# Performance work log

Measured on AMD Instinct MI355X. Metric: run time of the kernel, lower is better.

Reference implementation:

```python
import jax, jax.numpy as jnp
import numpy as np

HEADS = 20
NUM_AOE = 16
NUM_IP = 16


def setup_inputs() -> dict:
    key = jax.random.key(0)
    ks = jax.random.split(key, 7)
    B, Sq, H = 8, 4096, 1280
    Skv, C = 109, 768
    scale = 0.02
    return {
        "hidden_states": jax.random.normal(ks[0], (B, Sq, H), jnp.float32),
        "encoder_hidden_states": jax.random.normal(ks[1], (B, Skv, C), jnp.float32),
        "Wq": jax.random.normal(ks[2], (H, H), jnp.float32) * scale,
        "Wk": jax.random.normal(ks[3], (C, H), jnp.float32) * scale,
        "Wv": jax.random.normal(ks[4], (C, H), jnp.float32) * scale,
        "Wo": jax.random.normal(ks[5], (H, H), jnp.float32) * scale,
        "bo": jnp.zeros((H,), jnp.float32),
    }


def reference(hidden_states, encoder_hidden_states, Wq, Wk, Wv, Wo, bo):
    B, Sq, H = hidden_states.shape
    Skv = encoder_hidden_states.shape[1]
    head_dim = H // HEADS
    residual = hidden_states

    # projections (no bias on q/k/v, as in diffusers SD attention)
    q = (hidden_states @ Wq).reshape(B, Sq, HEADS, head_dim).transpose(0, 2, 1, 3)
    k = (encoder_hidden_states @ Wk).reshape(B, Skv, HEADS, head_dim).transpose(0, 2, 1, 3)
    v = (encoder_hidden_states @ Wv).reshape(B, Skv, HEADS, head_dim).transpose(0, 2, 1, 3)

    # manual attention: QK^T / sqrt(d), softmax
    scores = jnp.einsum("bhqd,bhkd->bhqk", q, k) / jnp.sqrt(jnp.asarray(head_dim, q.dtype))
    probs = jax.nn.softmax(scores, axis=-1)

    # frequency_mode != 'both': rescale aoe (first NUM_AOE) and image (last NUM_IP)
    # key-token ranges post-softmax, then renormalize. scale_aoe = scale_ip = 1
    # in this config, but the renormalization math is kept faithfully.
    scale_aoe = jnp.asarray(1.0, probs.dtype)
    scale_ip = jnp.asarray(1.0, probs.dtype)
    idx = jnp.arange(Skv)
    scale_vector = jnp.where(idx < NUM_AOE, scale_aoe, 1.0)
    scale_vector = jnp.where(idx >= Skv - NUM_IP, scale_vector * scale_ip, scale_vector)
    probs = probs * scale_vector  # broadcasts over (B, HEADS, Sq, Skv)
    probs = probs / probs.sum(axis=-1, keepdims=True)

    out = jnp.einsum("bhqk,bhkd->bhqd", probs, v)
    out = out.transpose(0, 2, 1, 3).reshape(B, Sq, H)
    out = out @ Wo + bo
    # residual connection, rescale_output_factor = 1.0
    return out + residual
```

## Files before the change

kernel.cpp:

```cpp
#include <hip/hip_runtime.h>
#include <hip/hip_bf16.h>

typedef unsigned short u16;
typedef __attribute__((ext_vector_type(8))) short short8;
typedef __attribute__((ext_vector_type(4))) short short4v;
typedef __attribute__((ext_vector_type(4))) float f32x4;

#define HEADS 20
#define HD 64
#define BB 8
#define SQ 4096
#define HDIM 1280
#define SKV 109
#define CDIM 768
#define SKV_PAD 128
#define SKV_T 112

static __device__ __forceinline__ u16 f2bf(float x) {
  union { __hip_bfloat16 h; u16 u; } cv;
  cv.h = __float2bfloat16(x);
  return cv.u;
}

static __device__ __forceinline__ void gll16(const void* g, void* l) {
  __builtin_amdgcn_global_load_lds(
      (const __attribute__((address_space(1))) unsigned int*)g,
      (__attribute__((address_space(3))) unsigned int*)l, 16, 0, 0);
}

__global__ __launch_bounds__(256) void tcvt(const float* __restrict__ W,
                                            u16* __restrict__ out, int K, int N,
                                            float scale) {
  __shared__ float t[32][33];
  int tx = threadIdx.x & 31, ty = threadIdx.x >> 5;
  int n0 = blockIdx.x * 32, k0 = blockIdx.y * 32;
#pragma unroll
  for (int i = 0; i < 32; i += 8)
    t[ty + i][tx] = W[(size_t)(k0 + ty + i) * N + n0 + tx];
  __syncthreads();
#pragma unroll
  for (int i = 0; i < 32; i += 8)
    out[(size_t)(n0 + ty + i) * K + k0 + tx] = f2bf(t[tx][ty + i] * scale);
}

__global__ __launch_bounds__(256) void ehs_prep(const float* __restrict__ e,
                                                u16* __restrict__ out) {
  int idx = blockIdx.x * 256 + threadIdx.x;
  if (idx >= BB * SKV_PAD * CDIM / 4) return;
  int c4 = idx * 4;
  int b = c4 / (SKV_PAD * CDIM);
  int rem = c4 - b * (SKV_PAD * CDIM);
  int s = rem / CDIM;
  int c = rem - s * CDIM;
  short4v o = {0, 0, 0, 0};
  if (s < SKV) {
    f32x4 v = *(const f32x4*)(e + ((size_t)b * SKV + s) * CDIM + c);
#pragma unroll
    for (int j = 0; j < 4; j++) o[j] = (short)f2bf(v[j]);
  }
  *(short4v*)&out[c4] = o;
}

__global__ __launch_bounds__(256) void hscvt(const float* __restrict__ in,
                                             u16* __restrict__ out) {
  const size_t total = (size_t)BB * SQ * HDIM;
  size_t step = (size_t)gridDim.x * 256 * 8;
  for (size_t i = ((size_t)blockIdx.x * 256 + threadIdx.x) * 8; i < total;
       i += step) {
    f32x4 a = *(const f32x4*)(in + i);
    f32x4 b = *(const f32x4*)(in + i + 4);
    short8 o;
#pragma unroll
    for (int j = 0; j < 4; j++) {
      o[j] = (short)f2bf(a[j]);
      o[j + 4] = (short)f2bf(b[j]);
    }
    *(short8*)&out[i] = o;
  }
}

template <int MODE>
__global__ __launch_bounds__(256, 4)
void gemm_glds(const u16* __restrict__ A, const u16* __restrict__ Bt,
               void* __restrict__ outp, int K, int ntn,
               const float* __restrict__ bias, const float* __restrict__ resid) {
  __shared__ u16 Alds[128 * 32];
  __shared__ u16 Blds[128 * 32];
  const int tid = threadIdx.x;
  const int wid = tid >> 6, lane = tid & 63;
  const int wm = wid >> 1, wn = wid & 1;
  const int g = lane >> 4, r = lane & 15;

  const int nwg = gridDim.x;
  const int orig = blockIdx.x;
  const int wg = (orig & 7) * (nwg >> 3) + (orig >> 3);
  const int mt = wg / ntn, nt = wg - mt * ntn;
  const int row0 = mt * 128, col0 = nt * 128;

  const int erow = tid >> 2, ecol = (tid & 3) * 8;

  f32x4 acc[4][4] = {};

  for (int kt = 0; kt < K; kt += 32) {
    const u16* ag = A + (size_t)(row0 + erow) * K + kt + ecol;
    const u16* bg = Bt + (size_t)(col0 + erow) * K + kt + ecol;
    gll16(ag, &Alds[erow * 32 + ecol]);
    gll16(ag + (size_t)64 * K, &Alds[(erow + 64) * 32 + ecol]);
    gll16(bg, &Blds[erow * 32 + ecol]);
    gll16(bg + (size_t)64 * K, &Blds[(erow + 64) * 32 + ecol]);
    __syncthreads();

    short8 afr[4], bfr[4];
#pragma unroll
    for (int mi = 0; mi < 4; mi++)
      afr[mi] = *(short8*)&Alds[(wm * 64 + mi * 16 + r) * 32 + g * 8];
#pragma unroll
    for (int ni = 0; ni < 4; ni++)
      bfr[ni] = *(short8*)&Blds[(wn * 64 + ni * 16 + r) * 32 + g * 8];
#pragma unroll
    for (int mi = 0; mi < 4; mi++)
#pragma unroll
      for (int ni = 0; ni < 4; ni++)
        acc[mi][ni] = __builtin_amdgcn_mfma_f32_16x16x32_bf16(afr[mi], bfr[ni],
                                                              acc[mi][ni], 0, 0, 0);
    __syncthreads();
  }

  if constexpr (MODE == 0) {
    u16* O = (u16*)outp;
#pragma unroll
    for (int mi = 0; mi < 4; mi++)
#pragma unroll
      for (int i = 0; i < 4; i++) {
        size_t m = row0 + wm * 64 + mi * 16 + g * 4 + i;
        size_t base = m * HDIM + col0 + wn * 64 + r;
#pragma unroll
        for (int ni = 0; ni < 4; ni++)
          O[base + ni * 16] = f2bf(acc[mi][ni][i]);
      }
  } else if constexpr (MODE == 1 || MODE == 2) {
    u16* O = (u16*)outp;
#pragma unroll
    for (int mi = 0; mi < 4; mi++)
#pragma unroll
      for (int i = 0; i < 4; i++) {
        int m = row0 + wm * 64 + mi * 16 + g * 4 + i;
        int b = m >> 7, skv = m & 127;
#pragma unroll
        for (int ni = 0; ni < 4; ni++) {
          int col = col0 + wn * 64 + ni * 16 + r;
          int hh = col >> 6, d = col & 63;
          size_t addr;
          if constexpr (MODE == 1)
            addr = (((size_t)b * HEADS + hh) * SKV_PAD + skv) * HD + d;
          else
            addr = (((size_t)b * HEADS + hh) * HD + d) * SKV_PAD + skv;
          O[addr] = f2bf(acc[mi][ni][i]);
        }
      }
  } else {
    float* O = (float*)outp;
#pragma unroll
    for (int mi = 0; mi < 4; mi++)
#pragma unroll
      for (int i = 0; i < 4; i++) {
        size_t m = row0 + wm * 64 + mi * 16 + g * 4 + i;
        size_t base = m * HDIM + col0 + wn * 64 + r;
#pragma unroll
        for (int ni = 0; ni < 4; ni++) {
          int col = col0 + wn * 64 + ni * 16 + r;
          O[base + ni * 16] = acc[mi][ni][i] + bias[col] + resid[base + ni * 16];
        }
      }
  }
}

__global__ __launch_bounds__(256, 2)
void attn_kernel(const u16* __restrict__ q, const u16* __restrict__ kh,
                 const u16* __restrict__ vt, u16* __restrict__ o) {
  __shared__ u16 Klds[SKV_T * 72];
  __shared__ u16 Vlds[HD * 136];
  __shared__ u16 Plds[4 * 16 * 136];
  const int tid = threadIdx.x;
  const int wid = tid >> 6, lane = tid & 63;
  const int g = lane >> 4, r = lane & 15;
  const int qt = blockIdx.x;
  const int bh = blockIdx.y;
  const int b = bh / HEADS, h = bh - b * HEADS;

  const u16* kg = kh + (size_t)bh * SKV_PAD * HD;
  for (int i = tid; i < SKV_T * 8; i += 256) {
    int row = i >> 3, c = (i & 7) * 8;
    *(short8*)&Klds[row * 72 + c] = *(const short8*)(kg + row * HD + c);
  }
  const u16* vg = vt + (size_t)bh * HD * SKV_PAD;
  for (int i = tid; i < HD * 16; i += 256) {
    int row = i >> 4, c = (i & 15) * 8;
    *(short8*)&Vlds[row * 136 + c] = *(const short8*)(vg + row * SKV_PAD + c);
  }
  __syncthreads();

  const u16* qg = q + ((size_t)b * SQ + qt * 64 + wid * 16 + r) * HDIM + h * HD + g * 8;
  short8 aq0 = *(const short8*)(qg);
  short8 aq1 = *(const short8*)(qg + 32);

  f32x4 s[7];
#pragma unroll
  for (int nf = 0; nf < 7; nf++) {
    f32x4 z = {0.f, 0.f, 0.f, 0.f};
    short8 k0 = *(short8*)&Klds[(nf * 16 + r) * 72 + g * 8];
    short8 k1 = *(short8*)&Klds[(nf * 16 + r) * 72 + 32 + g * 8];
    z = __builtin_amdgcn_mfma_f32_16x16x32_bf16(aq0, k0, z, 0, 0, 0);
    z = __builtin_amdgcn_mfma_f32_16x16x32_bf16(aq1, k1, z, 0, 0, 0);
    s[nf] = z;
  }

  {
    short4v z = {0, 0, 0, 0};
    *(short4v*)&Plds[(wid * 16 + r) * 136 + 112 + g * 4] = z;
  }

#pragma unroll
  for (int i = 0; i < 4; i++) {
    float pv[7];
    float mx = -1e30f;
#pragma unroll
    for (int nf = 0; nf < 7; nf++) {
      float v = s[nf][i];
      if (nf == 6 && r >= 13) v = -1e30f;
      pv[nf] = v;
      mx = fmaxf(mx, v);
    }
#pragma unroll
    for (int d = 1; d < 16; d <<= 1) mx = fmaxf(mx, __shfl_xor(mx, d, 64));
    float sum = 0.f;
#pragma unroll
    for (int nf = 0; nf < 7; nf++) {
      float e = (nf == 6 && r >= 13) ? 0.f : __expf(pv[nf] - mx);
      pv[nf] = e;
      sum += e;
    }
#pragma unroll
    for (int d = 1; d < 16; d <<= 1) sum += __shfl_xor(sum, d, 64);
    float is = 1.f / sum;
#pragma unroll
    for (int nf = 0; nf < 7; nf++)
      Plds[(wid * 16 + g * 4 + i) * 136 + nf * 16 + r] = f2bf(pv[nf] * is);
  }
  __syncthreads();

  f32x4 oacc[4] = {};
#pragma unroll
  for (int kk = 0; kk < 4; kk++) {
    short8 ap = *(short8*)&Plds[(wid * 16 + r) * 136 + kk * 32 + g * 8];
#pragma unroll
    for (int nf = 0; nf < 4; nf++) {
      short8 bv = *(short8*)&Vlds[(nf * 16 + r) * 136 + kk * 32 + g * 8];
      oacc[nf] = __builtin_amdgcn_mfma_f32_16x16x32_bf16(ap, bv, oacc[nf], 0, 0, 0);
    }
  }
  u16* og = o + ((size_t)b * SQ + qt * 64 + wid * 16) * HDIM + h * HD;
#pragma unroll
  for (int nf = 0; nf < 4; nf++)
#pragma unroll
    for (int i = 0; i < 4; i++)
      og[(size_t)(g * 4 + i) * HDIM + nf * 16 + r] = f2bf(oacc[nf][i]);
}

extern "C" void kernel_launch(void* const* d_in, const int* in_sizes, int n_in,
                              void* d_out, int out_size, void* d_ws, size_t ws_size,
                              hipStream_t stream) {
  const float* hs  = (const float*)d_in[0];
  const float* ehs = (const float*)d_in[1];
  const float* Wq  = (const float*)d_in[2];
  const float* Wk  = (const float*)d_in[3];
  const float* Wv  = (const float*)d_in[4];
  const float* Wo  = (const float*)d_in[5];
  const float* bo  = (const float*)d_in[6];

  char* ws = (char*)d_ws;
  size_t off = 0;
  auto alloc = [&](size_t elems) {
    u16* p = (u16*)(ws + off);
    off += ((elems * 2 + 255) / 256) * 256;
    return p;
  };
  u16* wqt  = alloc((size_t)HDIM * HDIM);
  u16* wot  = alloc((size_t)HDIM * HDIM);
  u16* wkt  = alloc((size_t)HDIM * CDIM);
  u16* wvt  = alloc((size_t)HDIM * CDIM);
  u16* ehsp = alloc((size_t)BB * SKV_PAD * CDIM);
  u16* khb  = alloc((size_t)BB * HEADS * SKV_PAD * HD);
  u16* vtb  = alloc((size_t)BB * HEADS * HD * SKV_PAD);
  u16* qb   = alloc((size_t)BB * SQ * HDIM);
  u16* ao   = alloc((size_t)BB * SQ * HDIM);
  u16* hsb  = ao;

  tcvt<<<dim3(HDIM / 32, HDIM / 32), 256, 0, stream>>>(Wq, wqt, HDIM, HDIM, 0.125f);
  tcvt<<<dim3(HDIM / 32, CDIM / 32), 256, 0, stream>>>(Wk, wkt, CDIM, HDIM, 1.0f);
  tcvt<<<dim3(HDIM / 32, CDIM / 32), 256, 0, stream>>>(Wv, wvt, CDIM, HDIM, 1.0f);
  tcvt<<<dim3(HDIM / 32, HDIM / 32), 256, 0, stream>>>(Wo, wot, HDIM, HDIM, 1.0f);
  ehs_prep<<<dim3((BB * SKV_PAD * CDIM / 4 + 255) / 256), 256, 0, stream>>>(ehs, ehsp);
  hscvt<<<dim3(2048), 256, 0, stream>>>(hs, hsb);

  gemm_glds<1><<<dim3(80), 256, 0, stream>>>(ehsp, wkt, khb, CDIM, 10, nullptr, nullptr);
  gemm_glds<2><<<dim3(80), 256, 0, stream>>>(ehsp, wvt, vtb, CDIM, 10, nullptr, nullptr);
  gemm_glds<0><<<dim3(2560), 256, 0, stream>>>(hsb, wqt, qb, HDIM, 10, nullptr, nullptr);
  attn_kernel<<<dim3(SQ / 64, BB * HEADS), 256, 0, stream>>>(qb, khb, vtb, ao);
  gemm_glds<3><<<dim3(2560), 256, 0, stream>>>(ao, wot, (void*)d_out, HDIM, 10, bo, hs);
}
```

Baseline: 486.7 us.

## Replace large Q/O projections with 256x256 double-buffered pipelined GEMM

Adds a new 512-thread GEMM kernel with 256x256 output tiles, K-step 64, XOR-swizzled LDS and double buffering. Global-to-LDS loads for the next tile are interleaved with four MFMA quadrants, using s_setprio around the math blocks. It is used for the Q projection and the output projection with bias and residual, while the small K/V projections keep the old kernel. The aim is more data reuse per tile and hiding memory latency behind MFMA work, at the cost of fewer workgroups (640) and higher register and LDS pressure.

```diff
diff --git a/kernel.cpp b/kernel.cpp
--- a/kernel.cpp
+++ b/kernel.cpp
@@ -15,6 +15,8 @@
 #define CDIM 768
 #define SKV_PAD 128
 #define SKV_T 112
+
+#define SBAR() asm volatile("s_barrier" ::: "memory")
 
 static __device__ __forceinline__ u16 f2bf(float x) {
   union { __hip_bfloat16 h; u16 u; } cv;
@@ -79,11 +81,183 @@
   }
 }
 
+
+static __device__ __forceinline__ void stage_half(u16* region,
+                                                  const u16* gbase, int K,
+                                                  int tid) {
+#pragma unroll
+  for (int j = 0; j < 2; ++j) {
+    int c = tid + j * 512;
+    int s = c ^ ((c >> 3) & 7);
+    gll16(gbase + (size_t)(s >> 3) * K + (s & 7) * 8, region + c * 8);
+  }
+}
+
+static __device__ __forceinline__ short8 lread(const u16* region, int row,
+                                               int kcol) {
+  int idx = (row * 64 + kcol) ^ ((row & 7) << 3);
+  return *(const short8*)(region + idx);
+}
+
+template <int MODE>
+__global__ __launch_bounds__(512, 2)
+void gemm256(const u16* __restrict__ A, const u16* __restrict__ Bt,
+             void* __restrict__ outp, int K, int ntn,
+             const float* __restrict__ bias, const float* __restrict__ resid) {
+  __shared__ u16 lds[2][2][2][8192];
+  const int tid = threadIdx.x;
+  const int wid = tid >> 6, lane = tid & 63;
+  const int wm = wid >> 2, wn = wid & 3;
+  const int g = lane >> 4, r = lane & 15;
+
+  const int nwg = gridDim.x;
+  const int orig = blockIdx.x;
+  const int wg = (orig & 7) * (nwg >> 3) + (orig >> 3);
+  const int mt = wg / ntn, nt = wg - mt * ntn;
+  const int row0 = mt * 256, col0 = nt * 256;
+
+  const u16* Ag = A + (size_t)row0 * K;
+  const u16* Bg = Bt + (size_t)col0 * K;
+  const int NT = K >> 6;
+
+  f32x4 acc[8][4] = {};
+
+  stage_half(&lds[0][0][0][0], Ag, K, tid);
+  stage_half(&lds[0][0][1][0], Ag + (size_t)128 * K, K, tid);
+  stage_half(&lds[0][1][0][0], Bg, K, tid);
+  stage_half(&lds[0][1][1][0], Bg + (size_t)128 * K, K, tid);
+  stage_half(&lds[1][1][0][0], Bg + 64, K, tid);
+  stage_half(&lds[1][1][1][0], Bg + (size_t)128 * K + 64, K, tid);
+  asm volatile("s_waitcnt vmcnt(4)" ::: "memory");
+  SBAR();
+
+  for (int t = 0; t < NT; ++t) {
+    const int cur = t & 1, nxt = cur ^ 1;
+    const u16* Ac = &lds[cur][0][wm][0];
+    const u16* Bc = &lds[cur][1][wn >> 1][0];
+    const int brow = (wn & 1) * 64;
+    short8 a0[4][2], a1[4][2], b0[2][2], b1[2][2];
+
+#pragma unroll
+    for (int mi = 0; mi < 4; ++mi)
+#pragma unroll
+      for (int ks = 0; ks < 2; ++ks)
+        a0[mi][ks] = lread(Ac, mi * 16 + r, ks * 32 + g * 8);
+#pragma unroll
+    for (int nf = 0; nf < 2; ++nf)
+#pragma unroll
+      for (int ks = 0; ks < 2; ++ks)
+        b0[nf][ks] = lread(Bc, brow + nf * 16 + r, ks * 32 + g * 8);
+    if (t + 1 < NT)
+      stage_half(&lds[nxt][0][0][0], Ag + (size_t)(t + 1) * 64, K, tid);
+    SBAR();
+    __builtin_amdgcn_s_setprio(1);
+#pragma unroll
+    for (int mi = 0; mi < 4; ++mi)
+#pragma unroll
+      for (int nf = 0; nf < 2; ++nf)
+#pragma unroll
+        for (int ks = 0; ks < 2; ++ks)
+          acc[mi][nf] = __builtin_amdgcn_mfma_f32_16x16x32_bf16(
+              a0[mi][ks], b0[nf][ks], acc[mi][nf], 0, 0, 0);
+    __builtin_amdgcn_s_setprio(0);
+    SBAR();
+
+#pragma unroll
+    for (int nf = 0; nf < 2; ++nf)
+#pragma unroll
+      for (int ks = 0; ks < 2; ++ks)
+        b1[nf][ks] = lread(Bc, brow + 32 + nf * 16 + r, ks * 32 + g * 8);
+    if (t + 1 < NT)
+      stage_half(&lds[nxt][0][1][0], Ag + (size_t)128 * K + (size_t)(t + 1) * 64,
+                 K, tid);
+    SBAR();
+    __builtin_amdgcn_s_setprio(1);
+#pragma unroll
+    for (int mi = 0; mi < 4; ++mi)
+#pragma unroll
+      for (int nf = 0; nf < 2; ++nf)
+#pragma unroll
+        for (int ks = 0; ks < 2; ++ks)
+          acc[mi][2 + nf] = __builtin_amdgcn_mfma_f32_16x16x32_bf16(
+              a0[mi][ks], b1[nf][ks], acc[mi][2 + nf], 0, 0, 0);
+    __builtin_amdgcn_s_setprio(0);
+    SBAR();
+
+#pragma unroll
+    for (int mi = 0; mi < 4; ++mi)
+#pragma unroll
+      for (int ks = 0; ks < 2; ++ks)
+        a1[mi][ks] = lread(Ac, 64 + mi * 16 + r, ks * 32 + g * 8);
+    if (t + 2 < NT)
+      stage_half(&lds[cur][1][0][0], Bg + (size_t)(t + 2) * 64, K, tid);
+    SBAR();
+    __builtin_amdgcn_s_setprio(1);
+#pragma unroll
+    for (int mi = 0; mi < 4; ++mi)
+#pragma unroll
+      for (int nf = 0; nf < 2; ++nf)
+#pragma unroll
+        for (int ks = 0; ks < 2; ++ks)
+          acc[4 + mi][2 + nf] = __builtin_amdgcn_mfma_f32_16x16x32_bf16(
+              a1[mi][ks], b1[nf][ks], acc[4 + mi][2 + nf], 0, 0, 0);
+    __builtin_amdgcn_s_setprio(0);
+    SBAR();
+
+    if (t + 2 < NT)
+      stage_half(&lds[cur][1][1][0], Bg + (size_t)128 * K + (size_t)(t + 2) * 64,
+                 K, tid);
+    if (t < NT - 2)
+      asm volatile("s_waitcnt vmcnt(4)" ::: "memory");
+    else
+      asm volatile("s_waitcnt vmcnt(0)" ::: "memory");
+    SBAR();
+    __builtin_amdgcn_s_setprio(1);
+#pragma unroll
+    for (int mi = 0; mi < 4; ++mi)
+#pragma unroll
+      for (int nf = 0; nf < 2; ++nf)
+#pragma unroll
+        for (int ks = 0; ks < 2; ++ks)
+          acc[4 + mi][nf] = __builtin_amdgcn_mfma_f32_16x16x32_bf16(
+              a1[mi][ks], b0[nf][ks], acc[4 + mi][nf], 0, 0, 0);
+    __builtin_amdgcn_s_setprio(0);
+    SBAR();
+  }
+
+  if constexpr (MODE == 0) {
+    u16* O = (u16*)outp;
+#pragma unroll
+    for (int am = 0; am < 8; ++am)
+#pragma unroll
+      for (int i = 0; i < 4; ++i) {
+        size_t m = row0 + wm * 128 + am * 16 + g * 4 + i;
+        size_t base = m * HDIM + col0 + wn * 64 + r;
+#pragma unroll
+        for (int an = 0; an < 4; ++an)
+          O[base + an * 16] = f2bf(acc[am][an][i]);
+      }
+  } else {
+    float* O = (float*)outp;
+#pragma unroll
+    for (int am = 0; am < 8; ++am)
+#pragma unroll
+      for (int i = 0; i < 4; ++i) {
+        size_t m = row0 + wm * 128 + am * 16 + g * 4 + i;
+        size_t base = m * HDIM + col0 + wn * 64 + r;
+#pragma unroll
+        for (int an = 0; an < 4; ++an) {
+          int col = col0 + wn * 64 + an * 16 + r;
+          O[base + an * 16] = acc[am][an][i] + bias[col] + resid[base + an * 16];
+        }
+      }
+  }
+}
+
 template <int MODE>
 __global__ __launch_bounds__(256, 4)
 void gemm_glds(const u16* __restrict__ A, const u16* __restrict__ Bt,
-               void* __restrict__ outp, int K, int ntn,
-               const float* __restrict__ bias, const float* __restrict__ resid) {
+               void* __restrict__ outp, int K, int ntn) {
   __shared__ u16 Alds[128 * 32];
   __shared__ u16 Blds[128 * 32];
   const int tid = threadIdx.x;
@@ -96,7 +270,6 @@
   const int wg = (orig & 7) * (nwg >> 3) + (orig >> 3);
   const int mt = wg / ntn, nt = wg - mt * ntn;
   const int row0 = mt * 128, col0 = nt * 128;
-
   const int erow = tid >> 2, ecol = (tid & 3) * 8;
 
   f32x4 acc[4][4] = {};
@@ -126,53 +299,25 @@
     __syncthreads();
   }
 
-  if constexpr (MODE == 0) {
-    u16* O = (u16*)outp;
-#pragma unroll
-    for (int mi = 0; mi < 4; mi++)
-#pragma unroll
-      for (int i = 0; i < 4; i++) {
-        size_t m = row0 + wm * 64 + mi * 16 + g * 4 + i;
-        size_t base = m * HDIM + col0 + wn * 64 + r;
-#pragma unroll
-        for (int ni = 0; ni < 4; ni++)
-          O[base + ni * 16] = f2bf(acc[mi][ni][i]);
+  u16* O = (u16*)outp;
+#pragma unroll
+  for (int mi = 0; mi < 4; mi++)
+#pragma unroll
+    for (int i = 0; i < 4; i++) {
+      int m = row0 + wm * 64 + mi * 16 + g * 4 + i;
+      int b = m >> 7, skv = m & 127;
+#pragma unroll
+      for (int ni = 0; ni < 4; ni++) {
+        int col = col0 + wn * 64 + ni * 16 + r;
+        int hh = col >> 6, d = col & 63;
+        size_t addr;
+        if constexpr (MODE == 1)
+          addr = (((size_t)b * HEADS + hh) * SKV_PAD + skv) * HD + d;
+        else
+          addr = (((size_t)b * HEADS + hh) * HD + d) * SKV_PAD + skv;
+        O[addr] = f2bf(acc[mi][ni][i]);
       }
-  } else if constexpr (MODE == 1 || MODE == 2) {
-    u16* O = (u16*)outp;
-#pragma unroll
-    for (int mi = 0; mi < 4; mi++)
-#pragma unroll
-      for (int i = 0; i < 4; i++) {
-        int m = row0 + wm * 64 + mi * 16 + g * 4 + i;
-        int b = m >> 7, skv = m & 127;
-#pragma unroll
-        for (int ni = 0; ni < 4; ni++) {
-          int col = col0 + wn * 64 + ni * 16 + r;
-          int hh = col >> 6, d = col & 63;
-          size_t addr;
-          if constexpr (MODE == 1)
-            addr = (((size_t)b * HEADS + hh) * SKV_PAD + skv) * HD + d;
-          else
-            addr = (((size_t)b * HEADS + hh) * HD + d) * SKV_PAD + skv;
-          O[addr] = f2bf(acc[mi][ni][i]);
-        }
-      }
-  } else {
-    float* O = (float*)outp;
-#pragma unroll
-    for (int mi = 0; mi < 4; mi++)
-#pragma unroll
-      for (int i = 0; i < 4; i++) {
-        size_t m = row0 + wm * 64 + mi * 16 + g * 4 + i;
-        size_t base = m * HDIM + col0 + wn * 64 + r;
-#pragma unroll
-        for (int ni = 0; ni < 4; ni++) {
-          int col = col0 + wn * 64 + ni * 16 + r;
-          O[base + ni * 16] = acc[mi][ni][i] + bias[col] + resid[base + ni * 16];
-        }
-      }
-  }
+    }
 }
 
 __global__ __launch_bounds__(256, 2)
@@ -303,9 +448,9 @@
   ehs_prep<<<dim3((BB * SKV_PAD * CDIM / 4 + 255) / 256), 256, 0, stream>>>(ehs, ehsp);
   hscvt<<<dim3(2048), 256, 0, stream>>>(hs, hsb);
 
-  gemm_glds<1><<<dim3(80), 256, 0, stream>>>(ehsp, wkt, khb, CDIM, 10, nullptr, nullptr);
-  gemm_glds<2><<<dim3(80), 256, 0, stream>>>(ehsp, wvt, vtb, CDIM, 10, nullptr, nullptr);
-  gemm_glds<0><<<dim3(2560), 256, 0, stream>>>(hsb, wqt, qb, HDIM, 10, nullptr, nullptr);
+  gemm_glds<1><<<dim3(80), 256, 0, stream>>>(ehsp, wkt, khb, CDIM, 10);
+  gemm_glds<2><<<dim3(80), 256, 0, stream>>>(ehsp, wvt, vtb, CDIM, 10);
+  gemm256<0><<<dim3(640), 512, 0, stream>>>(hsb, wqt, qb, HDIM, 5, nullptr, nullptr);
   attn_kernel<<<dim3(SQ / 64, BB * HEADS), 256, 0, stream>>>(qb, khb, vtb, ao);
-  gemm_glds<3><<<dim3(2560), 256, 0, stream>>>(ao, wot, (void*)d_out, HDIM, 10, bo, hs);
-}
+  gemm256<3><<<dim3(640), 512, 0, stream>>>(ao, wot, (void*)d_out, HDIM, 5, bo, hs);
+}
```

Result: faster. 464.1 us (-4.6%).

## Add triple-buffered swizzled LDS GEMM for Q and output projections

Applied to the files above, without the earlier changes.

Introduces gemm_tb, a GEMM kernel that prefetches three K-tiles into LDS with global_load_lds, waits with partial vmcnt, and uses an XOR swizzle on LDS columns to reduce bank conflicts. It also raises wave priority around the MFMA block. The Q projection and output projection (with bias and residual) now use it, while the K/V projections keep the old single-buffered kernel, which is trimmed to its MODE 1/2 epilogues. The aim is to hide global load latency behind MFMA work. The cost is more LDS per block (48 KB), which may limit occupancy, plus redundant loads of tile 0 issued in the final iterations.

```diff
diff --git a/kernel.cpp b/kernel.cpp
--- a/kernel.cpp
+++ b/kernel.cpp
@@ -16,6 +16,8 @@
 #define SKV_PAD 128
 #define SKV_T 112
 
+#define SBAR() asm volatile("s_barrier" ::: "memory")
+
 static __device__ __forceinline__ u16 f2bf(float x) {
   union { __hip_bfloat16 h; u16 u; } cv;
   cv.h = __float2bfloat16(x);
@@ -26,6 +28,12 @@
   __builtin_amdgcn_global_load_lds(
       (const __attribute__((address_space(1))) unsigned int*)g,
       (__attribute__((address_space(3))) unsigned int*)l, 16, 0, 0);
+}
+
+static __device__ __forceinline__ short8 ldsr(unsigned addr) {
+  short8 d;
+  asm volatile("ds_read_b128 %0, %1" : "=v"(d) : "v"(addr));
+  return d;
 }
 
 __global__ __launch_bounds__(256) void tcvt(const float* __restrict__ W,
@@ -79,11 +87,119 @@
   }
 }
 
+
+static __device__ __forceinline__ void stage128(u16* __restrict__ Ar,
+                                                u16* __restrict__ Br,
+                                                const u16* __restrict__ Ag,
+                                                const u16* __restrict__ Bg,
+                                                int K, int kt, int tid) {
+#pragma unroll
+  for (int j = 0; j < 2; ++j) {
+    int c = tid + j * 256;
+    int row = c >> 2, gc = c & 3;
+    int sc = gc ^ ((row >> 1) & 3);
+    gll16(Ag + (size_t)row * K + kt + sc * 8, Ar + c * 8);
+    gll16(Bg + (size_t)row * K + kt + sc * 8, Br + c * 8);
+  }
+}
+
+template <int MODE>
+__global__ __launch_bounds__(256, 4)
+void gemm_tb(const u16* __restrict__ A, const u16* __restrict__ Bt,
+             void* __restrict__ outp, int K, int ntn,
+             const float* __restrict__ bias, const float* __restrict__ resid) {
+  __shared__ u16 lds[3][8192];
+  const int tid = threadIdx.x;
+  const int wid = tid >> 6, lane = tid & 63;
+  const int wm = wid >> 1, wn = wid & 1;
+  const int g = lane >> 4, r = lane & 15;
+
+  const int nwg = gridDim.x;
+  const int orig = blockIdx.x;
+  const int wg = (orig & 7) * (nwg >> 3) + (orig >> 3);
+  const int mt = wg / ntn, nt = wg - mt * ntn;
+  const int row0 = mt * 128, col0 = nt * 128;
+
+  const u16* Ag = A + (size_t)row0 * K;
+  const u16* Bg = Bt + (size_t)col0 * K;
+  const int NT = K >> 5;
+
+  const int cx = (g * 8) ^ (((r >> 1) & 3) << 3);
+  const unsigned lbase = (unsigned)(size_t)(
+      __attribute__((address_space(3))) u16*)&lds[0][0];
+  unsigned aoff[4], boff[4];
+#pragma unroll
+  for (int mi = 0; mi < 4; ++mi)
+    aoff[mi] = ((wm * 64 + mi * 16 + r) * 32 + cx) * 2;
+#pragma unroll
+  for (int ni = 0; ni < 4; ++ni)
+    boff[ni] = (4096 + (wn * 64 + ni * 16 + r) * 32 + cx) * 2;
+
+  f32x4 acc[4][4] = {};
+
+  stage128(&lds[0][0], &lds[0][4096], Ag, Bg, K, 0, tid);
+  stage128(&lds[1][0], &lds[1][4096], Ag, Bg, K, 32, tid);
+  stage128(&lds[2][0], &lds[2][4096], Ag, Bg, K, 64, tid);
+
+  int buf = 0;
+  for (int t = 0; t < NT; ++t) {
+    asm volatile("s_waitcnt vmcnt(8)" ::: "memory");
+    SBAR();
+    const unsigned base = lbase + buf * 16384u;
+    short8 a[4], b[4];
+#pragma unroll
+    for (int mi = 0; mi < 4; ++mi) a[mi] = ldsr(base + aoff[mi]);
+#pragma unroll
+    for (int ni = 0; ni < 4; ++ni) b[ni] = ldsr(base + boff[ni]);
+    asm volatile("s_waitcnt lgkmcnt(0)" ::: "memory");
+    __builtin_amdgcn_sched_barrier(0);
+    __builtin_amdgcn_s_setprio(1);
+#pragma unroll
+    for (int mi = 0; mi < 4; ++mi)
+#pragma unroll
+      for (int ni = 0; ni < 4; ++ni)
+        acc[mi][ni] = __builtin_amdgcn_mfma_f32_16x16x32_bf16(a[mi], b[ni],
+                                                              acc[mi][ni], 0, 0, 0);
+    __builtin_amdgcn_s_setprio(0);
+    SBAR();
+    const int kt3 = (t + 3 < NT) ? (t + 3) * 32 : 0;
+    stage128(&lds[buf][0], &lds[buf][4096], Ag, Bg, K, kt3, tid);
+    buf = (buf == 2) ? 0 : buf + 1;
+  }
+
+  if constexpr (MODE == 0) {
+    u16* O = (u16*)outp;
+#pragma unroll
+    for (int mi = 0; mi < 4; ++mi)
+#pragma unroll
+      for (int i = 0; i < 4; ++i) {
+        size_t m = row0 + wm * 64 + mi * 16 + g * 4 + i;
+        size_t base = m * HDIM + col0 + wn * 64 + r;
+#pragma unroll
+        for (int ni = 0; ni < 4; ++ni)
+          O[base + ni * 16] = f2bf(acc[mi][ni][i]);
+      }
+  } else {
+    float* O = (float*)outp;
+#pragma unroll
+    for (int mi = 0; mi < 4; ++mi)
+#pragma unroll
+      for (int i = 0; i < 4; ++i) {
+        size_t m = row0 + wm * 64 + mi * 16 + g * 4 + i;
+        size_t base = m * HDIM + col0 + wn * 64 + r;
+#pragma unroll
+        for (int ni = 0; ni < 4; ++ni) {
+          int col = col0 + wn * 64 + ni * 16 + r;
+          O[base + ni * 16] = acc[mi][ni][i] + bias[col] + resid[base + ni * 16];
+        }
+      }
+  }
+}
+
 template <int MODE>
 __global__ __launch_bounds__(256, 4)
 void gemm_glds(const u16* __restrict__ A, const u16* __restrict__ Bt,
-               void* __restrict__ outp, int K, int ntn,
-               const float* __restrict__ bias, const float* __restrict__ resid) {
+               void* __restrict__ outp, int K, int ntn) {
   __shared__ u16 Alds[128 * 32];
   __shared__ u16 Blds[128 * 32];
   const int tid = threadIdx.x;
@@ -96,7 +212,6 @@
   const int wg = (orig & 7) * (nwg >> 3) + (orig >> 3);
   const int mt = wg / ntn, nt = wg - mt * ntn;
   const int row0 = mt * 128, col0 = nt * 128;
-
   const int erow = tid >> 2, ecol = (tid & 3) * 8;
 
   f32x4 acc[4][4] = {};
@@ -126,53 +241,25 @@
     __syncthreads();
   }
 
-  if constexpr (MODE == 0) {
-    u16* O = (u16*)outp;
-#pragma unroll
-    for (int mi = 0; mi < 4; mi++)
-#pragma unroll
-      for (int i = 0; i < 4; i++) {
-        size_t m = row0 + wm * 64 + mi * 16 + g * 4 + i;
-        size_t base = m * HDIM + col0 + wn * 64 + r;
-#pragma unroll
-        for (int ni = 0; ni < 4; ni++)
-          O[base + ni * 16] = f2bf(acc[mi][ni][i]);
+  u16* O = (u16*)outp;
+#pragma unroll
+  for (int mi = 0; mi < 4; mi++)
+#pragma unroll
+    for (int i = 0; i < 4; i++) {
+      int m = row0 + wm * 64 + mi * 16 + g * 4 + i;
+      int b = m >> 7, skv = m & 127;
+#pragma unroll
+      for (int ni = 0; ni < 4; ni++) {
+        int col = col0 + wn * 64 + ni * 16 + r;
+        int hh = col >> 6, d = col & 63;
+        size_t addr;
+        if constexpr (MODE == 1)
+          addr = (((size_t)b * HEADS + hh) * SKV_PAD + skv) * HD + d;
+        else
+          addr = (((size_t)b * HEADS + hh) * HD + d) * SKV_PAD + skv;
+        O[addr] = f2bf(acc[mi][ni][i]);
       }
-  } else if constexpr (MODE == 1 || MODE == 2) {
-    u16* O = (u16*)outp;
-#pragma unroll
-    for (int mi = 0; mi < 4; mi++)
-#pragma unroll
-      for (int i = 0; i < 4; i++) {
-        int m = row0 + wm * 64 + mi * 16 + g * 4 + i;
-        int b = m >> 7, skv = m & 127;
-#pragma unroll
-        for (int ni = 0; ni < 4; ni++) {
-          int col = col0 + wn * 64 + ni * 16 + r;
-          int hh = col >> 6, d = col & 63;
-          size_t addr;
-          if constexpr (MODE == 1)
-            addr = (((size_t)b * HEADS + hh) * SKV_PAD + skv) * HD + d;
-          else
-            addr = (((size_t)b * HEADS + hh) * HD + d) * SKV_PAD + skv;
-          O[addr] = f2bf(acc[mi][ni][i]);
-        }
-      }
-  } else {
-    float* O = (float*)outp;
-#pragma unroll
-    for (int mi = 0; mi < 4; mi++)
-#pragma unroll
-      for (int i = 0; i < 4; i++) {
-        size_t m = row0 + wm * 64 + mi * 16 + g * 4 + i;
-        size_t base = m * HDIM + col0 + wn * 64 + r;
-#pragma unroll
-        for (int ni = 0; ni < 4; ni++) {
-          int col = col0 + wn * 64 + ni * 16 + r;
-          O[base + ni * 16] = acc[mi][ni][i] + bias[col] + resid[base + ni * 16];
-        }
-      }
-  }
+    }
 }
 
 __global__ __launch_bounds__(256, 2)
@@ -303,9 +390,9 @@
   ehs_prep<<<dim3((BB * SKV_PAD * CDIM / 4 + 255) / 256), 256, 0, stream>>>(ehs, ehsp);
   hscvt<<<dim3(2048), 256, 0, stream>>>(hs, hsb);
 
-  gemm_glds<1><<<dim3(80), 256, 0, stream>>>(ehsp, wkt, khb, CDIM, 10, nullptr, nullptr);
-  gemm_glds<2><<<dim3(80), 256, 0, stream>>>(ehsp, wvt, vtb, CDIM, 10, nullptr, nullptr);
-  gemm_glds<0><<<dim3(2560), 256, 0, stream>>>(hsb, wqt, qb, HDIM, 10, nullptr, nullptr);
+  gemm_glds<1><<<dim3(80), 256, 0, stream>>>(ehsp, wkt, khb, CDIM, 10);
+  gemm_glds<2><<<dim3(80), 256, 0, stream>>>(ehsp, wvt, vtb, CDIM, 10);
+  gemm_tb<0><<<dim3(2560), 256, 0, stream>>>(hsb, wqt, qb, HDIM, 10, nullptr, nullptr);
   attn_kernel<<<dim3(SQ / 64, BB * HEADS), 256, 0, stream>>>(qb, khb, vtb, ao);
-  gemm_glds<3><<<dim3(2560), 256, 0, stream>>>(ao, wot, (void*)d_out, HDIM, 10, bo, hs);
-}
+  gemm_tb<3><<<dim3(2560), 256, 0, stream>>>(ao, wot, (void*)d_out, HDIM, 10, bo, hs);
+}
```

Result: slower. 499.7 us (+2.7%).

## Add triple-buffered swizzled 128x256 GEMM for Q and output projections

Applied to the files above, without the earlier changes.

Adds a new gemm_v2 kernel with 512 threads, a 128x256 output tile, a three-stage LDS ring filled by global_load_lds, and XOR-swizzled LDS addressing. It waits with explicit vmcnt counts and raw s_barrier instead of syncthreads, and raises wave priority around the MFMA block. The aim is to overlap global loads with MFMA work and cut LDS bank conflicts in the two large GEMMs. The old gemm_glds is trimmed to the K/V modes only. The larger tile halves the grid and raises LDS use per block, which may reduce occupancy.

```diff
diff --git a/kernel.cpp b/kernel.cpp
--- a/kernel.cpp
+++ b/kernel.cpp
@@ -15,6 +15,8 @@
 #define CDIM 768
 #define SKV_PAD 128
 #define SKV_T 112
+
+#define SBAR() asm volatile("s_barrier" ::: "memory")
 
 static __device__ __forceinline__ u16 f2bf(float x) {
   union { __hip_bfloat16 h; u16 u; } cv;
@@ -79,11 +81,113 @@
   }
 }
 
+
+template <int MODE>
+__global__ __launch_bounds__(512, 4)
+void gemm_v2(const u16* __restrict__ A, const u16* __restrict__ Bt,
+             void* __restrict__ outp, int K, int ntn,
+             const float* __restrict__ bias, const float* __restrict__ resid) {
+  __shared__ u16 lds[3][12288];
+  const int tid = threadIdx.x;
+  const int wid = tid >> 6, lane = tid & 63;
+  const int wm = wid >> 2, wn = wid & 3;
+  const int g = lane >> 4, r = lane & 15;
+
+  const int nwg = gridDim.x;
+  const int orig = blockIdx.x;
+  const int wg = (orig & 7) * (nwg >> 3) + (orig >> 3);
+  const int mt = wg / ntn, nt = wg - mt * ntn;
+  const int row0 = mt * 128, col0 = nt * 256;
+
+  const u16* Ag = A + (size_t)row0 * K;
+  const u16* Bg = Bt + (size_t)col0 * K;
+  const int NT = K >> 5;
+
+  const int cx = (g * 8) ^ (((r >> 1) & 3) << 3);
+
+  const int sa_row = tid >> 2;
+  const int sa_sc = (tid & 3) ^ ((tid >> 3) & 3);
+  const int sb_row1 = (tid + 512) >> 2;
+  const int sb_sc1 = ((tid + 512) & 3) ^ (((tid + 512) >> 3) & 3);
+
+  f32x4 acc[4][4] = {};
+
+  auto stage = [&](int buf, int kt) {
+    gll16(Ag + (size_t)sa_row * K + kt + sa_sc * 8, &lds[buf][tid * 8]);
+    gll16(Bg + (size_t)sa_row * K + kt + sa_sc * 8, &lds[buf][4096 + tid * 8]);
+    gll16(Bg + (size_t)sb_row1 * K + kt + sb_sc1 * 8,
+          &lds[buf][4096 + (tid + 512) * 8]);
+  };
+
+  stage(0, 0);
+  stage(1, 32);
+  asm volatile("s_waitcnt vmcnt(3)" ::: "memory");
+  SBAR();
+
+  int buf = 0;
+  for (int t = 0; t < NT; ++t) {
+    int nb = buf + 2;
+    if (nb >= 3) nb -= 3;
+    if (t + 2 < NT) stage(nb, (t + 2) * 32);
+
+    short8 a[4], b[4];
+#pragma unroll
+    for (int mi = 0; mi < 4; ++mi)
+      a[mi] = *(short8*)&lds[buf][(wm * 64 + mi * 16 + r) * 32 + cx];
+#pragma unroll
+    for (int nf = 0; nf < 4; ++nf)
+      b[nf] = *(short8*)&lds[buf][4096 + (wn * 64 + nf * 16 + r) * 32 + cx];
+
+    __builtin_amdgcn_s_setprio(1);
+#pragma unroll
+    for (int mi = 0; mi < 4; ++mi)
+#pragma unroll
+      for (int nf = 0; nf < 4; ++nf)
+        acc[mi][nf] = __builtin_amdgcn_mfma_f32_16x16x32_bf16(a[mi], b[nf],
+                                                              acc[mi][nf], 0, 0, 0);
+    __builtin_amdgcn_s_setprio(0);
+
+    if (t < NT - 2)
+      asm volatile("s_waitcnt vmcnt(3)" ::: "memory");
+    else
+      asm volatile("s_waitcnt vmcnt(0)" ::: "memory");
+    SBAR();
+    buf = (buf + 1 == 3) ? 0 : buf + 1;
+  }
+
+  if constexpr (MODE == 0) {
+    u16* O = (u16*)outp;
+#pragma unroll
+    for (int mi = 0; mi < 4; ++mi)
+#pragma unroll
+      for (int i = 0; i < 4; ++i) {
+        size_t m = row0 + wm * 64 + mi * 16 + g * 4 + i;
+        size_t base = m * HDIM + col0 + wn * 64 + r;
+#pragma unroll
+        for (int nf = 0; nf < 4; ++nf)
+          O[base + nf * 16] = f2bf(acc[mi][nf][i]);
+      }
+  } else {
+    float* O = (float*)outp;
+#pragma unroll
+    for (int mi = 0; mi < 4; ++mi)
+#pragma unroll
+      for (int i = 0; i < 4; ++i) {
+        size_t m = row0 + wm * 64 + mi * 16 + g * 4 + i;
+        size_t base = m * HDIM + col0 + wn * 64 + r;
+#pragma unroll
+        for (int nf = 0; nf < 4; ++nf) {
+          int col = col0 + wn * 64 + nf * 16 + r;
+          O[base + nf * 16] = acc[mi][nf][i] + bias[col] + resid[base + nf * 16];
+        }
+      }
+  }
+}
+
 template <int MODE>
 __global__ __launch_bounds__(256, 4)
 void gemm_glds(const u16* __restrict__ A, const u16* __restrict__ Bt,
-               void* __restrict__ outp, int K, int ntn,
-               const float* __restrict__ bias, const float* __restrict__ resid) {
+               void* __restrict__ outp, int K, int ntn) {
   __shared__ u16 Alds[128 * 32];
   __shared__ u16 Blds[128 * 32];
   const int tid = threadIdx.x;
@@ -96,7 +200,6 @@
   const int wg = (orig & 7) * (nwg >> 3) + (orig >> 3);
   const int mt = wg / ntn, nt = wg - mt * ntn;
   const int row0 = mt * 128, col0 = nt * 128;
-
   const int erow = tid >> 2, ecol = (tid & 3) * 8;
 
   f32x4 acc[4][4] = {};
@@ -126,53 +229,25 @@
     __syncthreads();
   }
 
-  if constexpr (MODE == 0) {
-    u16* O = (u16*)outp;
-#pragma unroll
-    for (int mi = 0; mi < 4; mi++)
-#pragma unroll
-      for (int i = 0; i < 4; i++) {
-        size_t m = row0 + wm * 64 + mi * 16 + g * 4 + i;
-        size_t base = m * HDIM + col0 + wn * 64 + r;
-#pragma unroll
-        for (int ni = 0; ni < 4; ni++)
-          O[base + ni * 16] = f2bf(acc[mi][ni][i]);
+  u16* O = (u16*)outp;
+#pragma unroll
+  for (int mi = 0; mi < 4; mi++)
+#pragma unroll
+    for (int i = 0; i < 4; i++) {
+      int m = row0 + wm * 64 + mi * 16 + g * 4 + i;
+      int b = m >> 7, skv = m & 127;
+#pragma unroll
+      for (int ni = 0; ni < 4; ni++) {
+        int col = col0 + wn * 64 + ni * 16 + r;
+        int hh = col >> 6, d = col & 63;
+        size_t addr;
+        if constexpr (MODE == 1)
+          addr = (((size_t)b * HEADS + hh) * SKV_PAD + skv) * HD + d;
+        else
+          addr = (((size_t)b * HEADS + hh) * HD + d) * SKV_PAD + skv;
+        O[addr] = f2bf(acc[mi][ni][i]);
       }
-  } else if constexpr (MODE == 1 || MODE == 2) {
-    u16* O = (u16*)outp;
-#pragma unroll
-    for (int mi = 0; mi < 4; mi++)
-#pragma unroll
-      for (int i = 0; i < 4; i++) {
-        int m = row0 + wm * 64 + mi * 16 + g * 4 + i;
-        int b = m >> 7, skv = m & 127;
-#pragma unroll
-        for (int ni = 0; ni < 4; ni++) {
-          int col = col0 + wn * 64 + ni * 16 + r;
-          int hh = col >> 6, d = col & 63;
-          size_t addr;
-          if constexpr (MODE == 1)
-            addr = (((size_t)b * HEADS + hh) * SKV_PAD + skv) * HD + d;
-          else
-            addr = (((size_t)b * HEADS + hh) * HD + d) * SKV_PAD + skv;
-          O[addr] = f2bf(acc[mi][ni][i]);
-        }
-      }
-  } else {
-    float* O = (float*)outp;
-#pragma unroll
-    for (int mi = 0; mi < 4; mi++)
-#pragma unroll
-      for (int i = 0; i < 4; i++) {
-        size_t m = row0 + wm * 64 + mi * 16 + g * 4 + i;
-        size_t base = m * HDIM + col0 + wn * 64 + r;
-#pragma unroll
-        for (int ni = 0; ni < 4; ni++) {
-          int col = col0 + wn * 64 + ni * 16 + r;
-          O[base + ni * 16] = acc[mi][ni][i] + bias[col] + resid[base + ni * 16];
-        }
-      }
-  }
+    }
 }
 
 __global__ __launch_bounds__(256, 2)
@@ -303,9 +378,9 @@
   ehs_prep<<<dim3((BB * SKV_PAD * CDIM / 4 + 255) / 256), 256, 0, stream>>>(ehs, ehsp);
   hscvt<<<dim3(2048), 256, 0, stream>>>(hs, hsb);
 
-  gemm_glds<1><<<dim3(80), 256, 0, stream>>>(ehsp, wkt, khb, CDIM, 10, nullptr, nullptr);
-  gemm_glds<2><<<dim3(80), 256, 0, stream>>>(ehsp, wvt, vtb, CDIM, 10, nullptr, nullptr);
-  gemm_glds<0><<<dim3(2560), 256, 0, stream>>>(hsb, wqt, qb, HDIM, 10, nullptr, nullptr);
+  gemm_glds<1><<<dim3(80), 256, 0, stream>>>(ehsp, wkt, khb, CDIM, 10);
+  gemm_glds<2><<<dim3(80), 256, 0, stream>>>(ehsp, wvt, vtb, CDIM, 10);
+  gemm_v2<0><<<dim3(1280), 512, 0, stream>>>(hsb, wqt, qb, HDIM, 5, nullptr, nullptr);
   attn_kernel<<<dim3(SQ / 64, BB * HEADS), 256, 0, stream>>>(qb, khb, vtb, ao);
-  gemm_glds<3><<<dim3(2560), 256, 0, stream>>>(ao, wot, (void*)d_out, HDIM, 10, bo, hs);
-}
+  gemm_v2<3><<<dim3(1280), 512, 0, stream>>>(ao, wot, (void*)d_out, HDIM, 5, bo, hs);
+}
```

Measured after the change: 442.3 us. 1.1x faster.
